# Optimization experiments

Measured on AMD Instinct MI355X. Metric: run time of the kernel, lower is better.

## Reference

```python
import jax, jax.numpy as jnp
import numpy as np
import math

B, NQ, NS, K = 4, 4096, 16384, 16
P, IN, D = 3, 128, 256
H = D // 16   # nhead = out_dim // 16 = 16
HD = D // H   # head_dim = 16
RADIUS = 4.0
EPS = 1e-5


def _ln(x, g, b):
    m = jnp.mean(x, -1, keepdims=True)
    v = jnp.mean((x - m) ** 2, -1, keepdims=True)
    return (x - m) / jnp.sqrt(v + EPS) * g + b


def _pos_enc(x, W_pos, b_pos):
    # LearnablePositionalEncoding: cat([x, cos(Linear(2*pi*x))], -1)
    return jnp.concatenate([x, jnp.cos((2.0 * math.pi * x) @ W_pos + b_pos)], axis=-1)


def setup_inputs() -> dict:
    key = jax.random.key(0)
    ks = jax.random.split(key, 24)
    f32 = jnp.float32

    def w(k, shape):
        return jax.random.uniform(k, shape, f32, -1.0, 1.0) / np.float32(np.sqrt(shape[0]))

    inp = {}
    inp['q_pts'] = jax.random.normal(ks[0], (B, NQ, P), f32)
    inp['s_pts'] = jax.random.normal(ks[1], (B, NS, P), f32)
    inp['src_feats'] = jax.random.normal(ks[2], (B, NS, IN), f32)
    inp['query_feats'] = jax.random.normal(ks[3], (B, NQ, IN), f32)
    # shared proj (in_dim != out_dim, skip_dim=None -> skip_proj is the same Linear)
    inp['W_proj'] = w(ks[4], (IN, D)); inp['b_proj'] = jnp.zeros((D,), f32)
    # positional encoding Linear(p_dim, out_dim - p_dim)
    inp['W_pos'] = w(ks[5], (P, D - P)); inp['b_pos'] = jnp.zeros((D - P,), f32)
    # TransformerDecoderLayer (norm_first) params
    inp['ln1_g'] = jnp.ones((D,), f32); inp['ln1_b'] = jnp.zeros((D,), f32)
    inp['sa_Wv'] = w(ks[6], (D, D)); inp['sa_bv'] = jnp.zeros((D,), f32)
    inp['sa_Wo'] = w(ks[7], (D, D)); inp['sa_bo'] = jnp.zeros((D,), f32)
    inp['ln2_g'] = jnp.ones((D,), f32); inp['ln2_b'] = jnp.zeros((D,), f32)
    inp['ca_Wq'] = w(ks[8], (D, D)); inp['ca_bq'] = jnp.zeros((D,), f32)
    inp['ca_Wk'] = w(ks[9], (D, D)); inp['ca_bk'] = jnp.zeros((D,), f32)
    inp['ca_Wv'] = w(ks[10], (D, D)); inp['ca_bv'] = jnp.zeros((D,), f32)
    inp['ca_Wo'] = w(ks[11], (D, D)); inp['ca_bo'] = jnp.zeros((D,), f32)
    inp['ln3_g'] = jnp.ones((D,), f32); inp['ln3_b'] = jnp.zeros((D,), f32)
    inp['W1'] = w(ks[12], (D, D)); inp['b1'] = jnp.zeros((D,), f32)
    inp['W2'] = w(ks[13], (D, D)); inp['b2'] = jnp.zeros((D,), f32)
    inp['neighb_inds'] = jax.random.randint(ks[14], (B, NQ, K), 0, NS)
    return inp


def reference(q_pts, s_pts, src_feats, query_feats, W_proj, b_proj, W_pos, b_pos,
              ln1_g, ln1_b, sa_Wv, sa_bv, sa_Wo, sa_bo, ln2_g, ln2_b,
              ca_Wq, ca_bq, ca_Wk, ca_bk, ca_Wv, ca_bv, ca_Wo, ca_bo,
              ln3_g, ln3_b, W1, b1, W2, b2, neighb_inds):
    # append shadow point at 1e6 with zero feature row
    s_pts_ = jnp.concatenate([s_pts, jnp.full_like(s_pts[:, :1, :], 1e6)], axis=1)   # [B,NS+1,P]
    src_ = jnp.concatenate([src_feats, jnp.zeros_like(src_feats[:, :1, :])], axis=1)  # [B,NS+1,IN]
    src_p = src_ @ W_proj + b_proj            # proj(src_feats)  [B,NS+1,D]
    qf = query_feats @ W_proj + b_proj        # skip_proj == proj (skip_dim=None)
    inds = neighb_inds % (NS + 1)
    flat = inds.reshape(B, -1, 1)             # [B, NQ*K, 1]
    neighbors = jnp.take_along_axis(s_pts_, jnp.broadcast_to(flat, (B, NQ * K, P)), axis=1).reshape(B, NQ, K, P)
    neighb_x = jnp.take_along_axis(src_p, jnp.broadcast_to(flat, (B, NQ * K, D)), axis=1).reshape(B, NQ, K, D)
    neighbors = neighbors - q_pts[:, :, None, :]
    neighb_x = neighb_x + _pos_enc(neighbors / RADIUS, W_pos, b_pos)
    query_x = qf + _pos_enc(jnp.zeros_like(q_pts), W_pos, b_pos)
    mask = jnp.linalg.norm(neighbors, axis=-1) > RADIUS   # [B,NQ,K], True = invalid key

    x = query_x   # [B,NQ,D]: a length-1 target sequence per query point
    # --- self-attention block (seq len 1 -> softmax == 1 -> only V/O projections matter) ---
    h = _ln(x, ln1_g, ln1_b)
    x = x + (h @ sa_Wv + sa_bv) @ sa_Wo + sa_bo
    # --- cross-attention to K gathered neighbors ---
    h = _ln(x, ln2_g, ln2_b)
    q = (h @ ca_Wq + ca_bq).reshape(B, NQ, H, HD)
    kk = (neighb_x @ ca_Wk + ca_bk).reshape(B, NQ, K, H, HD)
    vv = (neighb_x @ ca_Wv + ca_bv).reshape(B, NQ, K, H, HD)
    scores = jnp.einsum('bnhd,bnkhd->bnhk', q, kk) / np.float32(np.sqrt(HD))
    scores = jnp.where(mask[:, :, None, :], jnp.float32(-1e9), scores)
    att = jax.nn.softmax(scores, axis=-1)
    ctx = jnp.einsum('bnhk,bnkhd->bnhd', att, vv).reshape(B, NQ, D)
    x = x + ctx @ ca_Wo + ca_bo
    # --- feed-forward (dim_feedforward == d_model, relu) ---
    h = _ln(x, ln3_g, ln3_b)
    x = x + jax.nn.relu(h @ W1 + b1) @ W2 + b2
    # original zeroes any NaNs (fully-masked rows); shapes chosen so this is a no-op
    return jnp.nan_to_num(x)
```

## Files before the change

kernel.cpp:

```cpp
#include <hip/hip_runtime.h>
#include <hip/hip_bf16.h>
#include <math.h>
#include <stdint.h>

typedef __attribute__((ext_vector_type(8))) short short8;
typedef __attribute__((ext_vector_type(4))) float floatx4;

#define DEVI __device__ __forceinline__

DEVI float b2f(unsigned short u) {
    union { unsigned int i; float f; } v; v.i = ((unsigned int)u) << 16; return v.f;
}
DEVI unsigned short f2b(float f) {
    unsigned int x = __float_as_uint(f);
    unsigned int r = (x + 0x7fffu + ((x >> 16) & 1u)) >> 16;
    return (unsigned short)r;
}

#define GLD16(gp, lp)                                                            \
    __builtin_amdgcn_global_load_lds(                                            \
        (__attribute__((address_space(1))) unsigned int*)(gp),                   \
        (__attribute__((address_space(3))) unsigned int*)(lp), 16, 0, 0)

static constexpr int NQ = 4096, NS = 16384;
static constexpr int NROW_Q = 4 * NQ;
static constexpr int NROW_S = 4 * NS;
static constexpr float INV2PI = 0.15915494309189535f;

__global__ void k_prep(const float* Wproj, const float* saWv, const float* saWo,
                       const float* caWq, const float* caWk, const float* caWv,
                       const float* caWo, const float* W1, const float* W2,
                       const float* b_pos,
                       unsigned short* wTproj, unsigned short* wTsaWv, unsigned short* wTsaWo,
                       unsigned short* wTcaWq, unsigned short* wTkv, unsigned short* wTcaWo,
                       unsigned short* wTW1, unsigned short* wTW2, float* penc0)
{
    int z = blockIdx.z;
    if (z == 9) {
        if (blockIdx.x == 0 && blockIdx.y == 0) {
            int c = threadIdx.y * 16 + threadIdx.x;
            float v = 0.f;
            if (c >= 3) {
                float rev = b_pos[c - 3] * INV2PI;
                rev -= floorf(rev);
                v = __builtin_amdgcn_cosf(rev);
            }
            penc0[c] = v;
        }
        return;
    }
    int n = blockIdx.x * 16 + threadIdx.x;
    int k = blockIdx.y * 16 + threadIdx.y;
    const float* src; unsigned short* dst; int K = 256;
    switch (z) {
        case 0: src = Wproj; dst = wTproj; K = 128; break;
        case 1: src = saWv;  dst = wTsaWv; break;
        case 2: src = saWo;  dst = wTsaWo; break;
        case 3: src = caWq;  dst = wTcaWq; break;
        case 4: src = caWk;  dst = wTkv;   break;
        case 5: src = caWv;  dst = wTkv + 256 * 256; break;
        case 6: src = caWo;  dst = wTcaWo; break;
        case 7: src = W1;    dst = wTW1;   break;
        default: src = W2;   dst = wTW2;   break;
    }
    if (k < K) dst[(size_t)n * K + k] = f2b(src[(size_t)k * 256 + n]);
}

__global__ void k_scale(const float* b_pos, float* bp2)
{
    int i = blockIdx.x * blockDim.x + threadIdx.x;
    if (i < 253) bp2[i] = b_pos[i] * INV2PI;
}

__global__ void k_cvt(const float* in, unsigned short* out, int n4)
{
    int i = blockIdx.x * blockDim.x + threadIdx.x;
    int stride = gridDim.x * blockDim.x;
    for (; i < n4; i += stride) {
        float4 v = ((const float4*)in)[i];
        unsigned long long p =
              (unsigned long long)f2b(v.x)
            | ((unsigned long long)f2b(v.y) << 16)
            | ((unsigned long long)f2b(v.z) << 32)
            | ((unsigned long long)f2b(v.w) << 48);
        ((unsigned long long*)out)[i] = p;
    }
}

template<int EPI>
__global__ __launch_bounds__(256, 2)
void k_gemm(const unsigned short* A, const unsigned short* BT, const float* bias,
            const float* extra, void* outp, int M, int N, int K)
{
    __shared__ alignas(16) unsigned short lA[128 * 64];
    __shared__ alignas(16) unsigned short lB[64 * 64];
    const int tid = threadIdx.x;
    const int wave = tid >> 6, lane = tid & 63;
    const int m0 = blockIdx.x * 128, n0 = blockIdx.y * 64;
    const int wm = (wave >> 1) * 64, wn = (wave & 1) * 32;
    floatx4 acc[4][2] = {};

    for (int kt = 0; kt < K; kt += 64) {
        __syncthreads();
        #pragma unroll
        for (int c = 0; c < 4; ++c) {
            int o = (tid + c * 256) * 16;
            int row = o >> 7, inner = o & 127;
            int srk = inner ^ ((row & 7) << 4);
            GLD16((const char*)A + ((size_t)(m0 + row) * K + kt) * 2 + srk, (char*)lA + o);
        }
        #pragma unroll
        for (int c = 0; c < 2; ++c) {
            int o = (tid + c * 256) * 16;
            int row = o >> 7, inner = o & 127;
            int srk = inner ^ ((row & 7) << 4);
            GLD16((const char*)BT + ((size_t)(n0 + row) * K + kt) * 2 + srk, (char*)lB + o);
        }
        __syncthreads();
        #pragma unroll
        for (int kc = 0; kc < 2; ++kc) {
            const int kb = kc * 64 + ((lane >> 4) << 4);
            short8 bf[2];
            #pragma unroll
            for (int nf = 0; nf < 2; ++nf) {
                int nn = wn + nf * 16 + (lane & 15);
                bf[nf] = *(const short8*)((const char*)lB + nn * 128 + (kb ^ ((nn & 7) << 4)));
            }
            #pragma unroll
            for (int mf = 0; mf < 4; ++mf) {
                int rr = wm + mf * 16 + (lane & 15);
                short8 af = *(const short8*)((const char*)lA + rr * 128 + (kb ^ ((rr & 7) << 4)));
                acc[mf][0] = __builtin_amdgcn_mfma_f32_16x16x32_bf16(af, bf[0], acc[mf][0], 0, 0, 0);
                acc[mf][1] = __builtin_amdgcn_mfma_f32_16x16x32_bf16(af, bf[1], acc[mf][1], 0, 0, 0);
            }
        }
    }
    #pragma unroll
    for (int mf = 0; mf < 4; ++mf)
        #pragma unroll
        for (int nf = 0; nf < 2; ++nf)
            #pragma unroll
            for (int r = 0; r < 4; ++r) {
                int row = m0 + wm + mf * 16 + ((lane >> 4) << 2) + r;
                int col = n0 + wn + nf * 16 + (lane & 15);
                float v = acc[mf][nf][r] + bias[col];
                if (EPI == 4) v += extra[(size_t)row * N + col];
                if (EPI == 1) v = fmaxf(v, 0.f);
                if (EPI == 4) {
                    if (isnan(v)) v = 0.f;
                    else if (isinf(v)) v = v > 0.f ? 3.402823466e38f : -3.402823466e38f;
                }
                if (EPI == 0 || EPI == 1)
                    ((unsigned short*)outp)[(size_t)row * N + col] = f2b(v);
                else
                    ((float*)outp)[(size_t)row * N + col] = v;
            }
}

template<int EPI2>
__global__ __launch_bounds__(256, 2)
void k_gemm_ln(const unsigned short* A, const unsigned short* BT, const float* bias,
               const float* extra, const float* lng, const float* lnb,
               float* outf, unsigned short* outb, int M, int K)
{
    __shared__ alignas(16) unsigned short lA[64 * 64];
    __shared__ alignas(16) unsigned short lB[256 * 64];
    const int tid = threadIdx.x, wave = tid >> 6, lane = tid & 63;
    const int l15 = lane & 15, lg = lane >> 4;
    const int m0 = blockIdx.x * 64;
    floatx4 acc[16] = {};

    for (int kt = 0; kt < K; kt += 64) {
        __syncthreads();
        #pragma unroll
        for (int c = 0; c < 2; ++c) {
            int o = (tid + c * 256) * 16;
            int row = o >> 7, inner = o & 127;
            int srk = inner ^ ((row & 7) << 4);
            GLD16((const char*)A + ((size_t)(m0 + row) * K + kt) * 2 + srk, (char*)lA + o);
        }
        #pragma unroll
        for (int c = 0; c < 8; ++c) {
            int o = (tid + c * 256) * 16;
            int row = o >> 7, inner = o & 127;
            int srk = inner ^ ((row & 7) << 4);
            GLD16((const char*)BT + ((size_t)row * K + kt) * 2 + srk, (char*)lB + o);
        }
        __syncthreads();
        #pragma unroll
        for (int kc = 0; kc < 2; ++kc) {
            const int kb = kc * 64 + (lg << 4);
            int rr = wave * 16 + l15;
            short8 af = *(const short8*)((const char*)lA + rr * 128 + (kb ^ ((rr & 7) << 4)));
            #pragma unroll
            for (int nf = 0; nf < 16; ++nf) {
                int nn = nf * 16 + l15;
                short8 bf = *(const short8*)((const char*)lB + nn * 128 + (kb ^ ((nn & 7) << 4)));
                acc[nf] = __builtin_amdgcn_mfma_f32_16x16x32_bf16(af, bf, acc[nf], 0, 0, 0);
            }
        }
    }

    #pragma unroll
    for (int nf = 0; nf < 16; ++nf) {
        int col = nf * 16 + l15;
        float bi = bias[col] + (EPI2 == 0 ? extra[col] : 0.f);
        #pragma unroll
        for (int r = 0; r < 4; ++r) {
            int row = m0 + wave * 16 + lg * 4 + r;
            float v = acc[nf][r] + bi;
            if (EPI2 == 1) v += extra[(size_t)row * 256 + col];
            acc[nf][r] = v;
            outf[(size_t)row * 256 + col] = v;
        }
    }
    float mean[4], inv[4];
    #pragma unroll
    for (int r = 0; r < 4; ++r) {
        float s = 0.f;
        #pragma unroll
        for (int nf = 0; nf < 16; ++nf) s += acc[nf][r];
        #pragma unroll
        for (int t = 1; t <= 8; t <<= 1) s += __shfl_xor(s, t);
        mean[r] = s * (1.f / 256.f);
        float q = 0.f;
        #pragma unroll
        for (int nf = 0; nf < 16; ++nf) { float d = acc[nf][r] - mean[r]; q += d * d; }
        #pragma unroll
        for (int t = 1; t <= 8; t <<= 1) q += __shfl_xor(q, t);
        inv[r] = 1.0f / sqrtf(q * (1.f / 256.f) + 1e-5f);
    }
    #pragma unroll
    for (int nf = 0; nf < 16; ++nf) {
        int col = nf * 16 + l15;
        float g = lng[col], b = lnb[col];
        #pragma unroll
        for (int r = 0; r < 4; ++r) {
            int row = m0 + wave * 16 + lg * 4 + r;
            outb[(size_t)row * 256 + col] = f2b((acc[nf][r] - mean[r]) * inv[r] * g + b);
        }
    }
}

__global__ __launch_bounds__(256, 4)
void k_attn(const unsigned short* srcp, const unsigned short* qb, const int* inds,
            const float* s_pts, const float* q_pts, const float* W_pos, const float* bp2,
            const unsigned short* wTkv, const float* bv, unsigned short* ctx)
{
    __shared__ alignas(16) unsigned short nx[64 * 256];
    __shared__ alignas(16) float att_lds[4 * 16 * 16];
    __shared__ alignas(16) unsigned short qls[4 * 256];
    __shared__ alignas(16) float dist_lds[64];
    const int tid = threadIdx.x, wave = tid >> 6, lane = tid & 63;
    const int qbase = blockIdx.x * 4;
    const int l15 = lane & 15, lg = lane >> 4;

    if (tid < 128)
        *(uint4*)&qls[tid * 8] = *(const uint4*)(qb + (size_t)qbase * 256 + tid * 8);

    float bvv[4];
    #pragma unroll
    for (int nf = 0; nf < 4; ++nf) bvv[nf] = bv[(wave * 4 + nf) * 16 + l15];

    {
        int r = tid >> 2, sub = tid & 3;
        int qi = qbase + (r >> 4);
        int bb = qi >> 12;
        int k = r & 15;
        int raw = inds[((size_t)qi << 4) + k];
        int idx = raw % (NS + 1); if (idx < 0) idx += NS + 1;
        bool shadow = (idx == NS);
        const int c0 = sub * 64;
        const unsigned short* srow = srcp + ((size_t)bb * NS + (shadow ? 0 : idx)) * 256 + c0;
        short8 sv[8];
        #pragma unroll
        for (int j = 0; j < 8; ++j) sv[j] = *(const short8*)(srow + j * 8);

        float px = q_pts[(size_t)qi * 3], py = q_pts[(size_t)qi * 3 + 1], pz = q_pts[(size_t)qi * 3 + 2];
        float sx, sy, sz;
        if (shadow) { sx = sy = sz = 1e6f; }
        else {
            const float* sp = s_pts + ((size_t)bb * NS + idx) * 3;
            sx = sp[0]; sy = sp[1]; sz = sp[2];
        }
        float tx = (sx - px) * 0.25f, ty = (sy - py) * 0.25f, tz = (sz - pz) * 0.25f;
        if (sub == 0) dist_lds[r] = tx * tx + ty * ty + tz * tz;

        #pragma unroll
        for (int cc = 0; cc < 64; cc += 8) {
            short8 vals;
            #pragma unroll
            for (int j = 0; j < 8; ++j) {
                int c = c0 + cc + j;
                float pe;
                if (c == 0) pe = tx;
                else if (c == 1) pe = ty;
                else if (c == 2) pe = tz;
                else {
                    int jj = c - 3;
                    float rev = fmaf(tx, W_pos[jj],
                                fmaf(ty, W_pos[253 + jj],
                                fmaf(tz, W_pos[506 + jj], bp2[jj])));
                    rev -= floorf(rev);
                    pe = __builtin_amdgcn_cosf(rev);
                }
                float sval = shadow ? 0.f : b2f((unsigned short)sv[cc / 8][j]);
                vals[j] = (short)f2b(sval + pe);
            }
            int byte = (c0 + cc) * 2;
            *(short8*)((char*)nx + r * 512 + (byte ^ ((r & 7) << 4))) = vals;
        }
    }
    __syncthreads();

    const int wn = wave * 64;
    floatx4 acc[4][4];

    #pragma unroll
    for (int mf = 0; mf < 4; ++mf)
        #pragma unroll
        for (int nf = 0; nf < 4; ++nf) acc[mf][nf] = floatx4{0.f, 0.f, 0.f, 0.f};

    #pragma unroll 2
    for (int kt = 0; kt < 8; ++kt) {
        const int kb = kt * 64 + (lg << 4);
        short8 bfr[4];
        #pragma unroll
        for (int nf = 0; nf < 4; ++nf) {
            int nn = wn + nf * 16 + l15;
            bfr[nf] = *(const short8*)((const char*)wTkv + (size_t)nn * 512 + kt * 64 + (lg << 4));
        }
        #pragma unroll
        for (int mf = 0; mf < 4; ++mf) {
            int rr = mf * 16 + l15;
            short8 af = *(const short8*)((const char*)nx + rr * 512 + (kb ^ ((rr & 7) << 4)));
            #pragma unroll
            for (int nf = 0; nf < 4; ++nf)
                acc[mf][nf] = __builtin_amdgcn_mfma_f32_16x16x32_bf16(af, bfr[nf], acc[mf][nf], 0, 0, 0);
        }
    }

    {
        #pragma unroll
        for (int mf = 0; mf < 4; ++mf) {
            float4 d4 = *(const float4*)&dist_lds[mf * 16 + lg * 4];
            float dd4[4] = {d4.x, d4.y, d4.z, d4.w};
            #pragma unroll
            for (int nf = 0; nf < 4; ++nf) {
                float qvv = b2f(qls[mf * 256 + (wave * 4 + nf) * 16 + l15]);
                float s[4];
                #pragma unroll
                for (int rr = 0; rr < 4; ++rr) s[rr] = acc[mf][nf][rr] * qvv;
                #pragma unroll
                for (int t = 1; t <= 8; t <<= 1)
                    #pragma unroll
                    for (int rr = 0; rr < 4; ++rr) s[rr] += __shfl_xor(s[rr], t);
                #pragma unroll
                for (int rr = 0; rr < 4; ++rr)
                    s[rr] = (dd4[rr] > 1.0f) ? -1e9f : s[rr] * 0.25f;
                float m = fmaxf(fmaxf(s[0], s[1]), fmaxf(s[2], s[3]));
                m = fmaxf(m, __shfl_xor(m, 16));
                m = fmaxf(m, __shfl_xor(m, 32));
                float p[4], su = 0.f;
                #pragma unroll
                for (int rr = 0; rr < 4; ++rr) { p[rr] = __expf(s[rr] - m); su += p[rr]; }
                su += __shfl_xor(su, 16);
                su += __shfl_xor(su, 32);
                float inv = __builtin_amdgcn_rcpf(su);
                if (l15 == 0) {
                    float4 a4 = {p[0] * inv, p[1] * inv, p[2] * inv, p[3] * inv};
                    *(float4*)&att_lds[(mf * 16 + wave * 4 + nf) * 16 + lg * 4] = a4;
                }
            }
        }
    }

    #pragma unroll
    for (int mf = 0; mf < 4; ++mf)
        #pragma unroll
        for (int nf = 0; nf < 4; ++nf) acc[mf][nf] = floatx4{0.f, 0.f, 0.f, 0.f};

    #pragma unroll 2
    for (int kt = 0; kt < 8; ++kt) {
        const int kb = kt * 64 + (lg << 4);
        short8 bfr[4];
        #pragma unroll
        for (int nf = 0; nf < 4; ++nf) {
            int nn = 256 + wn + nf * 16 + l15;
            bfr[nf] = *(const short8*)((const char*)wTkv + (size_t)nn * 512 + kt * 64 + (lg << 4));
        }
        #pragma unroll
        for (int mf = 0; mf < 4; ++mf) {
            int rr = mf * 16 + l15;
            short8 af = *(const short8*)((const char*)nx + rr * 512 + (kb ^ ((rr & 7) << 4)));
            #pragma unroll
            for (int nf = 0; nf < 4; ++nf)
                acc[mf][nf] = __builtin_amdgcn_mfma_f32_16x16x32_bf16(af, bfr[nf], acc[mf][nf], 0, 0, 0);
        }
    }

    {
        #pragma unroll
        for (int mf = 0; mf < 4; ++mf)
            #pragma unroll
            for (int nf = 0; nf < 4; ++nf) {
                float4 a4 = *(const float4*)&att_lds[(mf * 16 + wave * 4 + nf) * 16 + lg * 4];
                float o = a4.x * acc[mf][nf][0];
                o = fmaf(a4.y, acc[mf][nf][1], o);
                o = fmaf(a4.z, acc[mf][nf][2], o);
                o = fmaf(a4.w, acc[mf][nf][3], o);
                o += __shfl_xor(o, 16);
                o += __shfl_xor(o, 32);
                o += bvv[nf];
                if (lane < 16)
                    ctx[(size_t)(qbase + mf) * 256 + (wave * 4 + nf) * 16 + lane] = f2b(o);
            }
    }
}

extern "C" void kernel_launch(void* const* d_in, const int* in_sizes, int n_in,
                              void* d_out, int out_size, void* d_ws, size_t ws_size,
                              hipStream_t stream)
{
    const float* q_pts   = (const float*)d_in[0];
    const float* s_pts   = (const float*)d_in[1];
    const float* src_f   = (const float*)d_in[2];
    const float* query_f = (const float*)d_in[3];
    const float* W_proj  = (const float*)d_in[4];
    const float* b_proj  = (const float*)d_in[5];
    const float* W_pos   = (const float*)d_in[6];
    const float* b_pos   = (const float*)d_in[7];
    const float* ln1_g   = (const float*)d_in[8];
    const float* ln1_b   = (const float*)d_in[9];
    const float* sa_Wv   = (const float*)d_in[10];
    const float* sa_bv   = (const float*)d_in[11];
    const float* sa_Wo   = (const float*)d_in[12];
    const float* sa_bo   = (const float*)d_in[13];
    const float* ln2_g   = (const float*)d_in[14];
    const float* ln2_b   = (const float*)d_in[15];
    const float* ca_Wq   = (const float*)d_in[16];
    const float* ca_bq   = (const float*)d_in[17];
    const float* ca_Wk   = (const float*)d_in[18];
    const float* ca_Wv   = (const float*)d_in[20];
    const float* ca_bv   = (const float*)d_in[21];
    const float* ca_Wo   = (const float*)d_in[22];
    const float* ca_bo   = (const float*)d_in[23];
    const float* ln3_g   = (const float*)d_in[24];
    const float* ln3_b   = (const float*)d_in[25];
    const float* W1      = (const float*)d_in[26];
    const float* b1      = (const float*)d_in[27];
    const float* W2      = (const float*)d_in[28];
    const float* b2      = (const float*)d_in[29];
    const int*   inds    = (const int*)d_in[30];

    char* ws = (char*)d_ws;
    size_t off = 0;
    auto alloc = [&](size_t bytes) { char* p = ws + off; off += (bytes + 1023) & ~(size_t)1023; return p; };

    unsigned short* wTproj = (unsigned short*)alloc(256 * 128 * 2);
    unsigned short* wTsaWv = (unsigned short*)alloc(256 * 256 * 2);
    unsigned short* wTsaWo = (unsigned short*)alloc(256 * 256 * 2);
    unsigned short* wTcaWq = (unsigned short*)alloc(256 * 256 * 2);
    unsigned short* wTkv   = (unsigned short*)alloc(512 * 256 * 2);
    unsigned short* wTcaWo = (unsigned short*)alloc(256 * 256 * 2);
    unsigned short* wTW1   = (unsigned short*)alloc(256 * 256 * 2);
    unsigned short* wTW2   = (unsigned short*)alloc(256 * 256 * 2);
    float*          penc0  = (float*)alloc(256 * 4);
    float*          bp2    = (float*)alloc(256 * 4);
    unsigned short* srcb   = (unsigned short*)alloc((size_t)NROW_S * 128 * 2);
    unsigned short* qfb    = (unsigned short*)alloc((size_t)NROW_Q * 128 * 2);
    unsigned short* srcp   = (unsigned short*)alloc((size_t)NROW_S * 256 * 2);
    float*          qx     = (float*)alloc((size_t)NROW_Q * 256 * 4);
    unsigned short* hbuf   = (unsigned short*)alloc((size_t)NROW_Q * 256 * 2);
    unsigned short* tbuf   = (unsigned short*)alloc((size_t)NROW_Q * 256 * 2);
    float*          xbuf   = (float*)alloc((size_t)NROW_Q * 256 * 4);
    unsigned short* qbuf   = (unsigned short*)alloc((size_t)NROW_Q * 256 * 2);
    unsigned short* ctxbuf = (unsigned short*)alloc((size_t)NROW_Q * 256 * 2);
    float*          x2buf  = (float*)alloc((size_t)NROW_Q * 256 * 4);

    dim3 bl16(16, 16);
    k_prep<<<dim3(16, 16, 10), bl16, 0, stream>>>(
        W_proj, sa_Wv, sa_Wo, ca_Wq, ca_Wk, ca_Wv, ca_Wo, W1, W2, b_pos,
        wTproj, wTsaWv, wTsaWo, wTcaWq, wTkv, wTcaWo, wTW1, wTW2, penc0);
    k_scale<<<1, 256, 0, stream>>>(b_pos, bp2);

    k_cvt<<<1024, 256, 0, stream>>>(src_f, srcb, NROW_S * 128 / 4);
    k_cvt<<<1024, 256, 0, stream>>>(query_f, qfb, NROW_Q * 128 / 4);

    k_gemm<0><<<dim3(512, 4), 256, 0, stream>>>(srcb, wTproj, b_proj, nullptr, srcp, NROW_S, 256, 128);
    k_gemm_ln<0><<<256, 256, 0, stream>>>(qfb, wTproj, b_proj, penc0, ln1_g, ln1_b,
                                          qx, hbuf, NROW_Q, 128);

    k_gemm<0><<<dim3(128, 4), 256, 0, stream>>>(hbuf, wTsaWv, sa_bv, nullptr, tbuf, NROW_Q, 256, 256);
    k_gemm_ln<1><<<256, 256, 0, stream>>>(tbuf, wTsaWo, sa_bo, qx, ln2_g, ln2_b,
                                          xbuf, hbuf, NROW_Q, 256);

    k_gemm<0><<<dim3(128, 4), 256, 0, stream>>>(hbuf, wTcaWq, ca_bq, nullptr, qbuf, NROW_Q, 256, 256);
    k_attn<<<4096, 256, 0, stream>>>(srcp, qbuf, inds, s_pts, q_pts, W_pos, bp2, wTkv, ca_bv, ctxbuf);
    k_gemm_ln<1><<<256, 256, 0, stream>>>(ctxbuf, wTcaWo, ca_bo, xbuf, ln3_g, ln3_b,
                                          x2buf, hbuf, NROW_Q, 256);

    k_gemm<1><<<dim3(128, 4), 256, 0, stream>>>(hbuf, wTW1, b1, nullptr, tbuf, NROW_Q, 256, 256);
    k_gemm<4><<<dim3(128, 4), 256, 0, stream>>>(tbuf, wTW2, b2, x2buf, d_out, NROW_Q, 256, 256);

    (void)in_sizes; (void)n_in; (void)out_size; (void)ws_size;
}
```

Before: 387.8 us.

## Fold self-attention V/O weights into one matrix and shrink attention blocks

Precomputes Wv·Wo and the fused bias (bv·Wo + bo) on the device. This drops the separate self-attention value GEMM and its intermediate buffer, so the LN-fused GEMM now reads hbuf directly. Separately, the cross-attention kernel now uses 128-thread blocks covering 2 queries instead of 4, with each wave owning 128 output columns, which halves LDS per block and doubles the grid. Pre-multiplying the weights in fp32 and then rounding to bf16 changes numerics slightly, and the fused GEMM reads and writes the same buffer (hbuf).

```diff
diff --git a/kernel.cpp b/kernel.cpp
--- a/kernel.cpp
+++ b/kernel.cpp
@@ -70,6 +70,20 @@
 {
     int i = blockIdx.x * blockDim.x + threadIdx.x;
     if (i < 253) bp2[i] = b_pos[i] * INV2PI;
+}
+
+__global__ void k_wfuse(const float* Wv, const float* Wo, const float* bv, const float* bo,
+                        unsigned short* wTsa, float* bsa)
+{
+    int n = blockIdx.x, k = threadIdx.x;
+    float s = 0.f;
+    for (int c = 0; c < 256; ++c) s = fmaf(Wv[k * 256 + c], Wo[c * 256 + n], s);
+    wTsa[n * 256 + k] = f2b(s);
+    if (k == 0) {
+        float s2 = bo[n];
+        for (int c = 0; c < 256; ++c) s2 = fmaf(bv[c], Wo[c * 256 + n], s2);
+        bsa[n] = s2;
+    }
 }
 
 __global__ void k_cvt(const float* in, unsigned short* out, int n4)
@@ -242,25 +256,25 @@
     }
 }
 
-__global__ __launch_bounds__(256, 4)
+__global__ __launch_bounds__(128, 4)
 void k_attn(const unsigned short* srcp, const unsigned short* qb, const int* inds,
             const float* s_pts, const float* q_pts, const float* W_pos, const float* bp2,
             const unsigned short* wTkv, const float* bv, unsigned short* ctx)
 {
-    __shared__ alignas(16) unsigned short nx[64 * 256];
-    __shared__ alignas(16) float att_lds[4 * 16 * 16];
-    __shared__ alignas(16) unsigned short qls[4 * 256];
-    __shared__ alignas(16) float dist_lds[64];
+    __shared__ alignas(16) unsigned short nx[32 * 256];
+    __shared__ alignas(16) float att_lds[2 * 16 * 16];
+    __shared__ alignas(16) unsigned short qls[2 * 256];
+    __shared__ alignas(16) float dist_lds[32];
     const int tid = threadIdx.x, wave = tid >> 6, lane = tid & 63;
-    const int qbase = blockIdx.x * 4;
+    const int qbase = blockIdx.x * 2;
     const int l15 = lane & 15, lg = lane >> 4;
 
-    if (tid < 128)
+    if (tid < 64)
         *(uint4*)&qls[tid * 8] = *(const uint4*)(qb + (size_t)qbase * 256 + tid * 8);
 
-    float bvv[4];
-    #pragma unroll
-    for (int nf = 0; nf < 4; ++nf) bvv[nf] = bv[(wave * 4 + nf) * 16 + l15];
+    float bvv[8];
+    #pragma unroll
+    for (int nf = 0; nf < 8; ++nf) bvv[nf] = bv[(wave * 8 + nf) * 16 + l15];
 
     {
         int r = tid >> 2, sub = tid & 3;
@@ -313,41 +327,44 @@
     }
     __syncthreads();
 
-    const int wn = wave * 64;
-    floatx4 acc[4][4];
-
-    #pragma unroll
-    for (int mf = 0; mf < 4; ++mf)
-        #pragma unroll
-        for (int nf = 0; nf < 4; ++nf) acc[mf][nf] = floatx4{0.f, 0.f, 0.f, 0.f};
+    const int wn = wave * 128;
+    floatx4 acc[2][8];
+
+    #pragma unroll
+    for (int mf = 0; mf < 2; ++mf)
+        #pragma unroll
+        for (int nf = 0; nf < 8; ++nf) acc[mf][nf] = floatx4{0.f, 0.f, 0.f, 0.f};
 
     #pragma unroll 2
     for (int kt = 0; kt < 8; ++kt) {
         const int kb = kt * 64 + (lg << 4);
-        short8 bfr[4];
-        #pragma unroll
-        for (int nf = 0; nf < 4; ++nf) {
-            int nn = wn + nf * 16 + l15;
-            bfr[nf] = *(const short8*)((const char*)wTkv + (size_t)nn * 512 + kt * 64 + (lg << 4));
-        }
-        #pragma unroll
-        for (int mf = 0; mf < 4; ++mf) {
-            int rr = mf * 16 + l15;
-            short8 af = *(const short8*)((const char*)nx + rr * 512 + (kb ^ ((rr & 7) << 4)));
-            #pragma unroll
-            for (int nf = 0; nf < 4; ++nf)
-                acc[mf][nf] = __builtin_amdgcn_mfma_f32_16x16x32_bf16(af, bfr[nf], acc[mf][nf], 0, 0, 0);
+        #pragma unroll
+        for (int nfg = 0; nfg < 2; ++nfg) {
+            short8 bfr[4];
+            #pragma unroll
+            for (int j = 0; j < 4; ++j) {
+                int nn = wn + (nfg * 4 + j) * 16 + l15;
+                bfr[j] = *(const short8*)((const char*)wTkv + (size_t)nn * 512 + kt * 64 + (lg << 4));
+            }
+            #pragma unroll
+            for (int mf = 0; mf < 2; ++mf) {
+                int rr = mf * 16 + l15;
+                short8 af = *(const short8*)((const char*)nx + rr * 512 + (kb ^ ((rr & 7) << 4)));
+                #pragma unroll
+                for (int j = 0; j < 4; ++j)
+                    acc[mf][nfg * 4 + j] = __builtin_amdgcn_mfma_f32_16x16x32_bf16(af, bfr[j], acc[mf][nfg * 4 + j], 0, 0, 0);
+            }
         }
     }
 
     {
         #pragma unroll
-        for (int mf = 0; mf < 4; ++mf) {
+        for (int mf = 0; mf < 2; ++mf) {
             float4 d4 = *(const float4*)&dist_lds[mf * 16 + lg * 4];
             float dd4[4] = {d4.x, d4.y, d4.z, d4.w};
             #pragma unroll
-            for (int nf = 0; nf < 4; ++nf) {
-                float qvv = b2f(qls[mf * 256 + (wave * 4 + nf) * 16 + l15]);
+            for (int nf = 0; nf < 8; ++nf) {
+                float qvv = b2f(qls[mf * 256 + (wave * 8 + nf) * 16 + l15]);
                 float s[4];
                 #pragma unroll
                 for (int rr = 0; rr < 4; ++rr) s[rr] = acc[mf][nf][rr] * qvv;
@@ -369,42 +386,45 @@
                 float inv = __builtin_amdgcn_rcpf(su);
                 if (l15 == 0) {
                     float4 a4 = {p[0] * inv, p[1] * inv, p[2] * inv, p[3] * inv};
-                    *(float4*)&att_lds[(mf * 16 + wave * 4 + nf) * 16 + lg * 4] = a4;
+                    *(float4*)&att_lds[(mf * 16 + wave * 8 + nf) * 16 + lg * 4] = a4;
                 }
             }
         }
     }
 
     #pragma unroll
-    for (int mf = 0; mf < 4; ++mf)
-        #pragma unroll
-        for (int nf = 0; nf < 4; ++nf) acc[mf][nf] = floatx4{0.f, 0.f, 0.f, 0.f};
+    for (int mf = 0; mf < 2; ++mf)
+        #pragma unroll
+        for (int nf = 0; nf < 8; ++nf) acc[mf][nf] = floatx4{0.f, 0.f, 0.f, 0.f};
 
     #pragma unroll 2
     for (int kt = 0; kt < 8; ++kt) {
         const int kb = kt * 64 + (lg << 4);
-        short8 bfr[4];
-        #pragma unroll
-        for (int nf = 0; nf < 4; ++nf) {
-            int nn = 256 + wn + nf * 16 + l15;
-            bfr[nf] = *(const short8*)((const char*)wTkv + (size_t)nn * 512 + kt * 64 + (lg << 4));
-        }
-        #pragma unroll
-        for (int mf = 0; mf < 4; ++mf) {
-            int rr = mf * 16 + l15;
-            short8 af = *(const short8*)((const char*)nx + rr * 512 + (kb ^ ((rr & 7) << 4)));
-            #pragma unroll
-            for (int nf = 0; nf < 4; ++nf)
-                acc[mf][nf] = __builtin_amdgcn_mfma_f32_16x16x32_bf16(af, bfr[nf], acc[mf][nf], 0, 0, 0);
+        #pragma unroll
+        for (int nfg = 0; nfg < 2; ++nfg) {
+            short8 bfr[4];
+            #pragma unroll
+            for (int j = 0; j < 4; ++j) {
+                int nn = 256 + wn + (nfg * 4 + j) * 16 + l15;
+                bfr[j] = *(const short8*)((const char*)wTkv + (size_t)nn * 512 + kt * 64 + (lg << 4));
+            }
+            #pragma unroll
+            for (int mf = 0; mf < 2; ++mf) {
+                int rr = mf * 16 + l15;
+                short8 af = *(const short8*)((const char*)nx + rr * 512 + (kb ^ ((rr & 7) << 4)));
+                #pragma unroll
+                for (int j = 0; j < 4; ++j)
+                    acc[mf][nfg * 4 + j] = __builtin_amdgcn_mfma_f32_16x16x32_bf16(af, bfr[j], acc[mf][nfg * 4 + j], 0, 0, 0);
+            }
         }
     }
 
     {
         #pragma unroll
-        for (int mf = 0; mf < 4; ++mf)
-            #pragma unroll
-            for (int nf = 0; nf < 4; ++nf) {
-                float4 a4 = *(const float4*)&att_lds[(mf * 16 + wave * 4 + nf) * 16 + lg * 4];
+        for (int mf = 0; mf < 2; ++mf)
+            #pragma unroll
+            for (int nf = 0; nf < 8; ++nf) {
+                float4 a4 = *(const float4*)&att_lds[(mf * 16 + wave * 8 + nf) * 16 + lg * 4];
                 float o = a4.x * acc[mf][nf][0];
                 o = fmaf(a4.y, acc[mf][nf][1], o);
                 o = fmaf(a4.z, acc[mf][nf][2], o);
@@ -413,7 +433,7 @@
                 o += __shfl_xor(o, 32);
                 o += bvv[nf];
                 if (lane < 16)
-                    ctx[(size_t)(qbase + mf) * 256 + (wave * 4 + nf) * 16 + lane] = f2b(o);
+                    ctx[(size_t)(qbase + mf) * 256 + (wave * 8 + nf) * 16 + lane] = f2b(o);
             }
     }
 }
@@ -465,6 +485,8 @@
     unsigned short* wTcaWo = (unsigned short*)alloc(256 * 256 * 2);
     unsigned short* wTW1   = (unsigned short*)alloc(256 * 256 * 2);
     unsigned short* wTW2   = (unsigned short*)alloc(256 * 256 * 2);
+    unsigned short* wTsa   = (unsigned short*)alloc(256 * 256 * 2);
+    float*          bsa    = (float*)alloc(256 * 4);
     float*          penc0  = (float*)alloc(256 * 4);
     float*          bp2    = (float*)alloc(256 * 4);
     unsigned short* srcb   = (unsigned short*)alloc((size_t)NROW_S * 128 * 2);
@@ -483,6 +505,7 @@
         W_proj, sa_Wv, sa_Wo, ca_Wq, ca_Wk, ca_Wv, ca_Wo, W1, W2, b_pos,
         wTproj, wTsaWv, wTsaWo, wTcaWq, wTkv, wTcaWo, wTW1, wTW2, penc0);
     k_scale<<<1, 256, 0, stream>>>(b_pos, bp2);
+    k_wfuse<<<256, 256, 0, stream>>>(sa_Wv, sa_Wo, sa_bv, sa_bo, wTsa, bsa);
 
     k_cvt<<<1024, 256, 0, stream>>>(src_f, srcb, NROW_S * 128 / 4);
     k_cvt<<<1024, 256, 0, stream>>>(query_f, qfb, NROW_Q * 128 / 4);
@@ -491,12 +514,11 @@
     k_gemm_ln<0><<<256, 256, 0, stream>>>(qfb, wTproj, b_proj, penc0, ln1_g, ln1_b,
                                           qx, hbuf, NROW_Q, 128);
 
-    k_gemm<0><<<dim3(128, 4), 256, 0, stream>>>(hbuf, wTsaWv, sa_bv, nullptr, tbuf, NROW_Q, 256, 256);
-    k_gemm_ln<1><<<256, 256, 0, stream>>>(tbuf, wTsaWo, sa_bo, qx, ln2_g, ln2_b,
+    k_gemm_ln<1><<<256, 256, 0, stream>>>(hbuf, wTsa, bsa, qx, ln2_g, ln2_b,
                                           xbuf, hbuf, NROW_Q, 256);
 
     k_gemm<0><<<dim3(128, 4), 256, 0, stream>>>(hbuf, wTcaWq, ca_bq, nullptr, qbuf, NROW_Q, 256, 256);
-    k_attn<<<4096, 256, 0, stream>>>(srcp, qbuf, inds, s_pts, q_pts, W_pos, bp2, wTkv, ca_bv, ctxbuf);
+    k_attn<<<8192, 128, 0, stream>>>(srcp, qbuf, inds, s_pts, q_pts, W_pos, bp2, wTkv, ca_bv, ctxbuf);
     k_gemm_ln<1><<<256, 256, 0, stream>>>(ctxbuf, wTcaWo, ca_bo, xbuf, ln3_g, ln3_b,
                                           x2buf, hbuf, NROW_Q, 256);
 
```

Result: slower. 523.7 us (+35.0%).
